# Optimization experiments

Hardware: AMD Instinct MI355X
Metric: run time of the kernel (lower is better)

## Reference

```python
import jax, jax.numpy as jnp
import numpy as np

B, CIN, COUT, H, W = 2, 128, 128, 128, 256
KH, KW = 3, 3
CMID = 32  # COUT // low_factor


def setup_inputs() -> dict:
    key = jax.random.key(0)
    ks = jax.random.split(key, 7)
    x = jax.random.normal(ks[0], (B, CIN, H, W), jnp.float32)
    # torchvision deform_conv2d offset layout: [2*KH*KW, Ho, Wo], (dy, dx) per tap
    offset = jax.random.normal(ks[1], (2 * KH * KW, H, W), jnp.float32)
    weight = jax.random.normal(ks[2], (COUT, CIN, KH, KW), jnp.float32) * 0.05
    bias = jax.random.normal(ks[3], (COUT,), jnp.float32) * 0.01
    down_w = jax.random.normal(ks[4], (CMID, 2 * COUT), jnp.float32) * 0.05
    up_w = jax.random.normal(ks[5], (COUT, CMID), jnp.float32) * 0.05
    scale = jnp.float32(1.0)
    return dict(x=x, offset=offset, weight=weight, bias=bias,
                down_w=down_w, up_w=up_w, scale=scale)


def _deform_conv2d(x, offset, weight, bias):
    # stride=1, padding=1, dilation=1, groups=1 (matches init_conv config)
    Bn, C, Hh, Ww = x.shape
    Co, _, kh, kw = weight.shape
    K = kh * kw
    Ho, Wo = offset.shape[-2:]
    off = offset.reshape(K, 2, Ho, Wo)
    dy, dx = off[:, 0], off[:, 1]                      # [K, Ho, Wo]
    ki, kj = jnp.meshgrid(jnp.arange(kh), jnp.arange(kw), indexing='ij')
    ki = ki.reshape(K).astype(jnp.float32)
    kj = kj.reshape(K).astype(jnp.float32)
    i = jnp.arange(Ho, dtype=jnp.float32)
    j = jnp.arange(Wo, dtype=jnp.float32)
    PAD = 1.0
    py = i[None, :, None] - PAD + ki[:, None, None] + dy   # [K, Ho, Wo]
    px = j[None, None, :] - PAD + kj[:, None, None] + dx
    y0 = jnp.floor(py).astype(jnp.int32)
    x0 = jnp.floor(px).astype(jnp.int32)
    fy = py - y0.astype(py.dtype)
    fx = px - x0.astype(px.dtype)
    xf = x.reshape(Bn, C, Hh * Ww)

    def gather(yi, xi, w):
        # zero padding outside the image (torchvision semantics)
        valid = (yi >= 0) & (yi < Hh) & (xi >= 0) & (xi < Ww)
        yc = jnp.clip(yi, 0, Hh - 1)
        xc = jnp.clip(xi, 0, Ww - 1)
        idx = (yc * Ww + xc).reshape(-1)                   # [K*Ho*Wo]
        g = xf[:, :, idx].reshape(Bn, C, K, Ho, Wo)
        return g * (w * valid.astype(w.dtype))[None, None]

    val = gather(y0, x0, (1.0 - fy) * (1.0 - fx))
    val = val + gather(y0, x0 + 1, (1.0 - fy) * fx)
    val = val + gather(y0 + 1, x0, fy * (1.0 - fx))
    val = val + gather(y0 + 1, x0 + 1, fy * fx)
    out = jnp.einsum('bcnij,ocn->boij', val, weight.reshape(Co, C, K))
    return out + bias[None, :, None, None]


def reference(x, offset, weight, bias, down_w, up_w, scale):
    # h = original frozen conv (weights shared with the deform branch, ablation != wo_copy)
    h = jax.lax.conv_general_dilated(
        x, weight, window_strides=(1, 1), padding=[(1, 1), (1, 1)],
        dimension_numbers=('NCHW', 'OIHW', 'NCHW'))
    h = h + bias[None, :, None, None]
    dx = _deform_conv2d(x, offset, weight, bias)
    dx = jnp.concatenate([dx, h], axis=1)                  # mix == 'cat'
    lo = jnp.einsum('bcij,dc->bdij', dx, down_w)           # 1x1 conv_down
    up = jnp.einsum('bcij,dc->bdij', lo, up_w)             # 1x1 conv_up
    return h + scale * up
```

## Files before the change

kernel.cpp:

```cpp
#include <hip/hip_runtime.h>
#include <hip/hip_bf16.h>

typedef __attribute__((ext_vector_type(8))) short short8;
typedef __attribute__((ext_vector_type(8))) unsigned short ushort8;
typedef __attribute__((ext_vector_type(4))) float f32x4;
typedef __attribute__((ext_vector_type(4))) int int4v;
typedef __attribute__((ext_vector_type(4))) float float4v;
typedef __attribute__((ext_vector_type(2))) float float2v;
typedef __attribute__((ext_vector_type(4))) unsigned int uint4v;

#define HH 128
#define WW 256
#define CIN_ 128
#define COUT_ 128

__device__ __forceinline__ unsigned short f2bf(float f) {
  union { __hip_bfloat16 h; unsigned short u; } v;
  v.h = __float2bfloat16(f);
  return v.u;
}

__global__ __launch_bounds__(256) void k_pre1(
    const float* __restrict__ down_w, const float* __restrict__ weight,
    float* __restrict__ T,
    const float* __restrict__ x, unsigned short* __restrict__ xh,
    const float* __restrict__ offset, int4v* __restrict__ mo,
    float4v* __restrict__ mw) {
  __shared__ float tile[32 * 129];
  int bid = blockIdx.x;
  int tid = threadIdx.x;

  if (bid < 288) {
    int e = bid * 256 + tid;
    if (e >= 2 * 32 * 1152) return;
    int s = e / 36864, r = e % 36864, d = r / 1152, ck = r % 1152;
    float a = 0.f;
    #pragma unroll 4
    for (int p = 0; p < 128; ++p)
      a += down_w[d * 256 + s * 128 + p] * weight[p * 1152 + ck];
    T[e] = a;
  } else if (bid < 2336) {
    int idx = bid - 288;
    int b = idx >> 10, rem = idx & 1023;
    int y = rem >> 3, xg = (rem & 7) << 5;
    for (int it = tid; it < 32 * 128; it += 256) {
      int c = it >> 5, xi = it & 31;
      tile[xi * 129 + c] = x[(((size_t)b * 128 + c) * 128 + y) * 256 + xg + xi];
    }
    __syncthreads();
    for (int it = tid; it < 32 * 16; it += 256) {
      int xi = it >> 4, cs = it & 15;
      ushort8 v;
      #pragma unroll
      for (int e = 0; e < 8; ++e) v[e] = f2bf(tile[xi * 129 + cs * 8 + e]);
      *(ushort8*)(xh + (((size_t)b * 128 + y) * 256 + xg + xi) * 128 + cs * 8) = v;
    }
  } else {
    int e = (bid - 2336) * 256 + tid;
    if (e >= 9 * 128 * 256) return;
    int k = e >> 15, rem = e & 32767;
    int ii = rem >> 8, jj = rem & 255;
    float dy = offset[(2 * k) * 32768 + rem];
    float dx = offset[(2 * k + 1) * 32768 + rem];
    int ki = k / 3, kj = k % 3;
    float py = (float)(ii - 1 + ki) + dy;
    float px = (float)(jj - 1 + kj) + dx;
    float fy0 = floorf(py), fx0 = floorf(px);
    int y0 = (int)fy0, x0 = (int)fx0;
    float fy = py - fy0, fx = px - fx0;
    int ys[2] = {y0, y0 + 1};
    int xs_[2] = {x0, x0 + 1};
    float wy[2] = {1.f - fy, fy}, wx[2] = {1.f - fx, fx};
    int4v o;
    float4v w;
    #pragma unroll
    for (int cy = 0; cy < 2; ++cy) {
      #pragma unroll
      for (int cx = 0; cx < 2; ++cx) {
        int yy = ys[cy], xx = xs_[cx];
        bool valid = (yy >= 0) && (yy < HH) && (xx < WW) && (xx >= 0);
        int yc = min(max(yy, 0), HH - 1), xc = min(max(xx, 0), WW - 1);
        int off = (yc * WW + xc) * CIN_;
        float wv = valid ? wy[cy] * wx[cx] : 0.f;
        int ci = cy * 2 + cx;
        if (ci == 0) { o.x = off; w.x = wv; }
        else if (ci == 1) { o.y = off; w.y = wv; }
        else if (ci == 2) { o.z = off; w.z = wv; }
        else { o.w = off; w.w = wv; }
      }
    }
    mo[e] = o;
    mw[e] = w;
  }
}

__global__ __launch_bounds__(256) void k_pre2(
    const float* __restrict__ up_w, const float* __restrict__ weight,
    const float* __restrict__ T, const float* __restrict__ scale,
    unsigned short* __restrict__ wdef, unsigned short* __restrict__ wstd,
    const float* __restrict__ down_w, const float* __restrict__ bias,
    float* __restrict__ beff) {
  __shared__ float sd[32];
  int bid = blockIdx.x;
  int t = threadIdx.x;
  if (bid < 1152) {
    int e = bid * 256 + t;
    if (e >= 2 * 9 * 128 * 128) return;
    int s = e / 147456, r = e % 147456;
    int tap = r / 16384, o = (r / 128) % 128, c = r % 128;
    int ck = c * 9 + tap;
    const float* Ts = T + s * 36864;
    float a = 0.f;
    #pragma unroll
    for (int d = 0; d < 32; ++d) a += up_w[o * 32 + d] * Ts[d * 1152 + ck];
    float scl = scale[0];
    int idx = ((tap * 4 + (c >> 5)) * 128 + o) * 32 + (c & 31);
    if (s == 1) {
      wstd[idx] = f2bf(weight[o * 1152 + ck] + scl * a);
    } else {
      wdef[idx] = f2bf(scl * a);
    }
  } else {
    if (t < 32) {
      float a = 0.f;
      for (int p = 0; p < 128; ++p)
        a += (down_w[t * 256 + p] + down_w[t * 256 + 128 + p]) * bias[p];
      sd[t] = a;
    }
    __syncthreads();
    if (t < 128) {
      float a = 0.f;
      #pragma unroll
      for (int d = 0; d < 32; ++d) a += up_w[t * 32 + d] * sd[d];
      beff[t] = bias[t] + scale[0] * a;
    }
  }
}

__global__ __launch_bounds__(512, 4) void k_main(
    const unsigned short* __restrict__ xh,
    const int4v* __restrict__ mo, const float4v* __restrict__ mw,
    const unsigned short* __restrict__ wstd, const unsigned short* __restrict__ wdef,
    const float* __restrict__ beff, float* __restrict__ out) {
  __shared__ __align__(16) unsigned short sbuf[2][2][64 * 128];

  int orig = blockIdx.x;
  int t = ((orig & 7) << 6) + (orig >> 3);
  int b = t >> 8, ip = (t >> 2) & 63, j0 = (t & 3) << 6;
  int i0 = ip << 1;
  int tid = threadIdx.x;
  const unsigned short* xb = xh + (size_t)b * (HH * WW * CIN_);

  int wid = tid >> 6;
  bool producer = wid < 4;

  if (producer) {
    int slot = tid & 15, pg = tid >> 4;
    int ce = slot * 8;

    auto COMB = [&](uint4v* g, float4v w, int q, unsigned short* buf) {
      int p = q * 16 + pg;
      uint4v r;
      #pragma unroll
      for (int wi = 0; wi < 4; ++wi) {
        unsigned u0 = g[0][wi], u1 = g[1][wi], u2 = g[2][wi], u3 = g[3][wi];
        float2v f0 = {__builtin_bit_cast(float, u0 << 16), __builtin_bit_cast(float, u0 & 0xffff0000u)};
        float2v f1 = {__builtin_bit_cast(float, u1 << 16), __builtin_bit_cast(float, u1 & 0xffff0000u)};
        float2v f2 = {__builtin_bit_cast(float, u2 << 16), __builtin_bit_cast(float, u2 & 0xffff0000u)};
        float2v f3 = {__builtin_bit_cast(float, u3 << 16), __builtin_bit_cast(float, u3 & 0xffff0000u)};
        float2v s = w.x * f0 + w.y * f1 + w.z * f2 + w.w * f3;
        unsigned rr;
        asm("v_cvt_pk_bf16_f32 %0, %1, %2" : "=v"(rr) : "v"(s.x), "v"(s.y));
        r[wi] = rr;
      }
      *(uint4v*)((char*)buf + (p << 8) + ((slot ^ (p & 15)) << 4)) = r;
    };

    auto STAGE_DEF = [&](int tap, int i, unsigned short* buf) {
      int4v o;
      float4v wq0, wq1;
      uint4v g0[4], g1[4];
      int mbase = (tap * HH + i) * WW + j0 + pg;

      o = mo[mbase]; wq0 = mw[mbase];
      g0[0] = *(const uint4v*)(xb + o.x + ce);
      g0[1] = *(const uint4v*)(xb + o.y + ce);
      g0[2] = *(const uint4v*)(xb + o.z + ce);
      g0[3] = *(const uint4v*)(xb + o.w + ce);
      o = mo[mbase + 16]; wq1 = mw[mbase + 16];
      g1[0] = *(const uint4v*)(xb + o.x + ce);
      g1[1] = *(const uint4v*)(xb + o.y + ce);
      g1[2] = *(const uint4v*)(xb + o.z + ce);
      g1[3] = *(const uint4v*)(xb + o.w + ce);

      COMB(g0, wq0, 0, buf);
      o = mo[mbase + 32]; wq0 = mw[mbase + 32];
      g0[0] = *(const uint4v*)(xb + o.x + ce);
      g0[1] = *(const uint4v*)(xb + o.y + ce);
      g0[2] = *(const uint4v*)(xb + o.z + ce);
      g0[3] = *(const uint4v*)(xb + o.w + ce);
      COMB(g1, wq1, 1, buf);
      o = mo[mbase + 48]; wq1 = mw[mbase + 48];
      g1[0] = *(const uint4v*)(xb + o.x + ce);
      g1[1] = *(const uint4v*)(xb + o.y + ce);
      g1[2] = *(const uint4v*)(xb + o.z + ce);
      g1[3] = *(const uint4v*)(xb + o.w + ce);
      COMB(g0, wq0, 2, buf);
      COMB(g1, wq1, 3, buf);
    };

    auto STAGE_STD = [&](int tap, int i, unsigned short* buf) {
      int ki = tap / 3, kj = tap % 3;
      int gy = i - 1 + ki;
      bool oky = (unsigned)gy < (unsigned)HH;
      uint4v s[4];
      #pragma unroll
      for (int q = 0; q < 4; ++q) {
        int p = q * 16 + pg;
        int gx = j0 + p - 1 + kj;
        uint4v vv = {};
        if (oky && (unsigned)gx < (unsigned)WW)
          vv = *(const uint4v*)(xb + (size_t)(gy * WW + gx) * CIN_ + ce);
        s[q] = vv;
      }
      #pragma unroll
      for (int q = 0; q < 4; ++q) {
        int p = q * 16 + pg;
        *(uint4v*)((char*)buf + (p << 8) + ((slot ^ (p & 15)) << 4)) = s[q];
      }
    };

    STAGE_STD(0, i0, sbuf[0][0]);
    STAGE_STD(0, i0 + 1, sbuf[0][1]);
    __syncthreads();
    for (int v = 0; v < 18; ++v) {
      if (v < 17) {
        int nv = v + 1;
        if (nv & 1) {
          STAGE_DEF(nv >> 1, i0, sbuf[nv & 1][0]);
          STAGE_DEF(nv >> 1, i0 + 1, sbuf[nv & 1][1]);
        } else {
          STAGE_STD(nv >> 1, i0, sbuf[nv & 1][0]);
          STAGE_STD(nv >> 1, i0 + 1, sbuf[nv & 1][1]);
        }
      }
      __syncthreads();
    }
  } else {
    int lane = tid & 63;
    int cw = wid - 4;
    int obase = cw << 5;
    int lrow = lane & 15, lhi = lane >> 4;

    f32x4 acc[2][2][4] = {};

    __syncthreads();
    for (int v = 0; v < 18; ++v) {
      const unsigned short* wt = ((v & 1) ? wdef : wstd) + (size_t)(v >> 1) * 16384;
      short8 af[4][2];
      #pragma unroll
      for (int cc = 0; cc < 4; ++cc)
        #pragma unroll
        for (int am = 0; am < 2; ++am)
          af[cc][am] = *(const short8*)(wt + ((size_t)(cc * 128 + obase + am * 16 + lrow)) * 32 + lhi * 8);
      #pragma unroll
      for (int tile = 0; tile < 2; ++tile) {
        const unsigned short* cur = sbuf[v & 1][tile];
        #pragma unroll
        for (int cc = 0; cc < 4; ++cc) {
          short8 bfr[4];
          #pragma unroll
          for (int bn = 0; bn < 4; ++bn) {
            int pp = bn * 16 + lrow;
            bfr[bn] = *(const short8*)((const char*)cur + (pp << 8) +
                                       (((cc * 4 + lhi) ^ lrow) << 4));
          }
          #pragma unroll
          for (int am = 0; am < 2; ++am)
            #pragma unroll
            for (int bn = 0; bn < 4; ++bn)
              acc[tile][am][bn] = __builtin_amdgcn_mfma_f32_16x16x32_bf16(af[cc][am], bfr[bn], acc[tile][am][bn], 0, 0, 0);
        }
      }
      __syncthreads();
    }

    #pragma unroll
    for (int tile = 0; tile < 2; ++tile) {
      #pragma unroll
      for (int am = 0; am < 2; ++am) {
        #pragma unroll
        for (int bn = 0; bn < 4; ++bn) {
          int jg = j0 + bn * 16 + lrow;
          #pragma unroll
          for (int r = 0; r < 4; ++r) {
            int o = obase + am * 16 + lhi * 4 + r;
            out[(((size_t)b * COUT_ + o) * HH + (i0 + tile)) * WW + jg] =
                acc[tile][am][bn][r] + beff[o];
          }
        }
      }
    }
  }
}

extern "C" void kernel_launch(void* const* d_in, const int* in_sizes, int n_in,
                              void* d_out, int out_size, void* d_ws, size_t ws_size,
                              hipStream_t stream) {
  const float* x      = (const float*)d_in[0];
  const float* offset = (const float*)d_in[1];
  const float* weight = (const float*)d_in[2];
  const float* bias   = (const float*)d_in[3];
  const float* down_w = (const float*)d_in[4];
  const float* up_w   = (const float*)d_in[5];
  const float* scale  = (const float*)d_in[6];
  float* out = (float*)d_out;

  char* ws = (char*)d_ws;
  unsigned short* xh   = (unsigned short*)(ws);
  int4v* mo            = (int4v*)(ws + 16777216);
  float4v* mw          = (float4v*)(ws + 21495808);
  unsigned short* wstd = (unsigned short*)(ws + 26214400);
  unsigned short* wdef = (unsigned short*)(ws + 26509312);
  float* T             = (float*)(ws + 26804224);
  float* beff          = (float*)(ws + 27099136);

  k_pre1<<<dim3(3488), dim3(256), 0, stream>>>(down_w, weight, T, x, xh, offset, mo, mw);
  k_pre2<<<dim3(1153), dim3(256), 0, stream>>>(up_w, weight, T, scale, wdef, wstd, down_w, bias, beff);
  k_main<<<dim3(512), dim3(512), 0, stream>>>(xh, mo, mw, wstd, wdef, beff, out);
}
```

Measured before the change: 93.88 us.

## Stage a shared input halo window once for standard-conv taps

The producer warps now load a 4x66 pixel halo window of the bf16 input into shared memory once, instead of restaging a shifted 64-pixel tile for each of the nine standard-conv taps. The consumer warps read the standard taps straight from this window with tap-dependent offsets. The deformable taps keep a single buffer that is filled during the standard-tap iterations. This cuts redundant global loads and producer work but raises LDS use to about 100KB per block, which may lower occupancy. Deformable staging now overlaps only the standard-tap compute, so the pipelining is less even.

```diff
diff --git a/kernel.cpp b/kernel.cpp
--- a/kernel.cpp
+++ b/kernel.cpp
@@ -142,7 +142,8 @@
     const int4v* __restrict__ mo, const float4v* __restrict__ mw,
     const unsigned short* __restrict__ wstd, const unsigned short* __restrict__ wdef,
     const float* __restrict__ beff, float* __restrict__ out) {
-  __shared__ __align__(16) unsigned short sbuf[2][2][64 * 128];
+  __shared__ __align__(16) unsigned short win[4 * 66 * 128];
+  __shared__ __align__(16) unsigned short dbuf[2][64 * 128];
 
   int orig = blockIdx.x;
   int t = ((orig & 7) << 6) + (orig >> 3);
@@ -157,6 +158,16 @@
   if (producer) {
     int slot = tid & 15, pg = tid >> 4;
     int ce = slot * 8;
+
+    for (int it = tid; it < 4 * 66 * 16; it += 256) {
+      int s = it & 15, colr = it >> 4;
+      int c = colr % 66, r = colr / 66;
+      int gy = i0 - 1 + r, gx = j0 - 1 + c;
+      uint4v vv = {};
+      if ((unsigned)gy < (unsigned)HH && (unsigned)gx < (unsigned)WW)
+        vv = *(const uint4v*)(xb + (size_t)(gy * WW + gx) * CIN_ + s * 8);
+      *(uint4v*)((char*)win + ((r * 66 + c) << 8) + ((s ^ (c & 15)) << 4)) = vv;
+    }
 
     auto COMB = [&](uint4v* g, float4v w, int q, unsigned short* buf) {
       int p = q * 16 + pg;
@@ -209,40 +220,12 @@
       COMB(g1, wq1, 3, buf);
     };
 
-    auto STAGE_STD = [&](int tap, int i, unsigned short* buf) {
-      int ki = tap / 3, kj = tap % 3;
-      int gy = i - 1 + ki;
-      bool oky = (unsigned)gy < (unsigned)HH;
-      uint4v s[4];
-      #pragma unroll
-      for (int q = 0; q < 4; ++q) {
-        int p = q * 16 + pg;
-        int gx = j0 + p - 1 + kj;
-        uint4v vv = {};
-        if (oky && (unsigned)gx < (unsigned)WW)
-          vv = *(const uint4v*)(xb + (size_t)(gy * WW + gx) * CIN_ + ce);
-        s[q] = vv;
-      }
-      #pragma unroll
-      for (int q = 0; q < 4; ++q) {
-        int p = q * 16 + pg;
-        *(uint4v*)((char*)buf + (p << 8) + ((slot ^ (p & 15)) << 4)) = s[q];
-      }
-    };
-
-    STAGE_STD(0, i0, sbuf[0][0]);
-    STAGE_STD(0, i0 + 1, sbuf[0][1]);
     __syncthreads();
     for (int v = 0; v < 18; ++v) {
-      if (v < 17) {
-        int nv = v + 1;
-        if (nv & 1) {
-          STAGE_DEF(nv >> 1, i0, sbuf[nv & 1][0]);
-          STAGE_DEF(nv >> 1, i0 + 1, sbuf[nv & 1][1]);
-        } else {
-          STAGE_STD(nv >> 1, i0, sbuf[nv & 1][0]);
-          STAGE_STD(nv >> 1, i0 + 1, sbuf[nv & 1][1]);
-        }
+      if (!(v & 1) && v < 17) {
+        int tap = v >> 1;
+        STAGE_DEF(tap, i0, dbuf[0]);
+        STAGE_DEF(tap, i0 + 1, dbuf[1]);
       }
       __syncthreads();
     }
@@ -263,23 +246,48 @@
         #pragma unroll
         for (int am = 0; am < 2; ++am)
           af[cc][am] = *(const short8*)(wt + ((size_t)(cc * 128 + obase + am * 16 + lrow)) * 32 + lhi * 8);
-      #pragma unroll
-      for (int tile = 0; tile < 2; ++tile) {
-        const unsigned short* cur = sbuf[v & 1][tile];
+
+      if (v & 1) {
         #pragma unroll
-        for (int cc = 0; cc < 4; ++cc) {
-          short8 bfr[4];
+        for (int tile = 0; tile < 2; ++tile) {
+          const unsigned short* cur = dbuf[tile];
           #pragma unroll
-          for (int bn = 0; bn < 4; ++bn) {
-            int pp = bn * 16 + lrow;
-            bfr[bn] = *(const short8*)((const char*)cur + (pp << 8) +
-                                       (((cc * 4 + lhi) ^ lrow) << 4));
+          for (int cc = 0; cc < 4; ++cc) {
+            short8 bfr[4];
+            #pragma unroll
+            for (int bn = 0; bn < 4; ++bn) {
+              int pp = bn * 16 + lrow;
+              bfr[bn] = *(const short8*)((const char*)cur + (pp << 8) +
+                                         (((cc * 4 + lhi) ^ lrow) << 4));
+            }
+            #pragma unroll
+            for (int am = 0; am < 2; ++am)
+              #pragma unroll
+              for (int bn = 0; bn < 4; ++bn)
+                acc[tile][am][bn] = __builtin_amdgcn_mfma_f32_16x16x32_bf16(af[cc][am], bfr[bn], acc[tile][am][bn], 0, 0, 0);
           }
+        }
+      } else {
+        int tap = v >> 1;
+        int ki = tap / 3, kj = tap % 3;
+        #pragma unroll
+        for (int tile = 0; tile < 2; ++tile) {
+          int wrow = tile + ki;
           #pragma unroll
-          for (int am = 0; am < 2; ++am)
+          for (int cc = 0; cc < 4; ++cc) {
+            short8 bfr[4];
             #pragma unroll
-            for (int bn = 0; bn < 4; ++bn)
-              acc[tile][am][bn] = __builtin_amdgcn_mfma_f32_16x16x32_bf16(af[cc][am], bfr[bn], acc[tile][am][bn], 0, 0, 0);
+            for (int bn = 0; bn < 4; ++bn) {
+              int wcol = bn * 16 + lrow + kj;
+              bfr[bn] = *(const short8*)((const char*)win + ((wrow * 66 + wcol) << 8) +
+                                         (((cc * 4 + lhi) ^ (wcol & 15)) << 4));
+            }
+            #pragma unroll
+            for (int am = 0; am < 2; ++am)
+              #pragma unroll
+              for (int bn = 0; bn < 4; ++bn)
+                acc[tile][am][bn] = __builtin_amdgcn_mfma_f32_16x16x32_bf16(af[cc][am], bfr[bn], acc[tile][am][bn], 0, 0, 0);
+          }
         }
       }
       __syncthreads();
```

After: 116.6 us. 1.24x slower.
